# Performance work log

Hardware: AMD Instinct MI355X
Metric: run time of the kernel (lower is better)

Reference implementation:

```python
import jax, jax.numpy as jnp
import numpy as np

N = 100000      # nodes
E = 1600000     # edges (avg degree 16)
DIN = 32
DOUT = 32


def setup_inputs() -> dict:
    key = jax.random.key(0)
    k1, k2, k3 = jax.random.split(key, 3)
    x = jax.random.normal(k1, (N, DIN), dtype=jnp.float32)
    edge_index = jax.random.randint(k2, (2, E), 0, N)  # [2, E] (src, dst)
    W = jax.random.normal(k3, (DIN, DOUT), dtype=jnp.float32) / np.sqrt(DIN).astype(np.float32)
    b = jnp.zeros((DOUT,), dtype=jnp.float32)
    return {"x": x, "edge_index": edge_index, "W": W, "b": b}


def reference(x, edge_index, W, b):
    # GCNConv with norm='both' (DGL GraphConv semantics):
    # out = D_dst^{-1/2} * A * (D_src^{-1/2} * X * W) + b
    src, dst = edge_index[0], edge_index[1]
    ones = jnp.ones((edge_index.shape[1],), dtype=x.dtype)
    out_deg = jax.ops.segment_sum(ones, src, num_segments=N)  # out-degree of src nodes
    in_deg = jax.ops.segment_sum(ones, dst, num_segments=N)   # in-degree of dst nodes
    norm_src = jnp.where(out_deg > 0, out_deg ** -0.5, 0.0)   # [N]
    norm_dst = jnp.where(in_deg > 0, in_deg ** -0.5, 0.0)     # [N]
    # feature transform before aggregation (in_feats >= out_feats path)
    h = (x * norm_src[:, None]) @ W                           # [N, DOUT]
    # sparse neighbor aggregation: gather along src, scatter-add to dst
    agg = jax.ops.segment_sum(h[src], dst, num_segments=N)    # [N, DOUT]
    return agg * norm_dst[:, None] + b
```

## Files before the change

kernel.cpp:

```cpp
#include <hip/hip_runtime.h>
#include <hip/hip_bf16.h>

#define DIN 32
#define DOUT 32
#define BINSHIFT 8
#define BINW 256
#define NBMAX 512
#define PTHREADS 512
#define PK 8
#define PB (PTHREADS * PK)
#define SRCBITS 17
#define SRCMASK ((1u << SRCBITS) - 1u)
#define CAP_LDS 8192
#define AK (CAP_LDS / 1024)

__device__ __forceinline__ float bf_lo(unsigned v) { return __uint_as_float(v << 16); }
__device__ __forceinline__ float bf_hi(unsigned v) { return __uint_as_float(v & 0xffff0000u); }
__device__ __forceinline__ unsigned f2bf_rne(float f) {
    unsigned u = __float_as_uint(f);
    return (u + 0x7fffu + ((u >> 16) & 1u)) >> 16;
}

__global__ void init_caps_kernel(int* __restrict__ baseS, int* __restrict__ baseD,
                                 int* __restrict__ curS, int* __restrict__ curD,
                                 int NB, int cap) {
    int i = threadIdx.x;
    if (i <= NB) {
        int v = i * cap;
        baseS[i] = v; baseD[i] = v;
        if (i < NB) { curS[i] = v; curD[i] = v; }
    }
}

__global__ void hist_coarse_kernel(const int* __restrict__ src, const int* __restrict__ dst,
                                   int E, int* __restrict__ gcntS, int* __restrict__ gcntD) {
    __shared__ int hS[NBMAX], hD[NBMAX];
    for (int i = threadIdx.x; i < NBMAX; i += 256) { hS[i] = 0; hD[i] = 0; }
    __syncthreads();
    int stride = gridDim.x * blockDim.x;
    for (int e = blockIdx.x * blockDim.x + threadIdx.x; e < E; e += stride) {
        atomicAdd(&hS[src[e] >> BINSHIFT], 1);
        atomicAdd(&hD[dst[e] >> BINSHIFT], 1);
    }
    __syncthreads();
    for (int i = threadIdx.x; i < NBMAX; i += 256) {
        if (hS[i]) atomicAdd(&gcntS[i], hS[i]);
        if (hD[i]) atomicAdd(&gcntD[i], hD[i]);
    }
}

__global__ void scan_coarse_kernel(const int* __restrict__ gcntS, const int* __restrict__ gcntD,
                                   int* __restrict__ baseS, int* __restrict__ baseD,
                                   int* __restrict__ curS, int* __restrict__ curD,
                                   int NB, int E) {
    __shared__ int s1[NBMAX], s2[NBMAX];
    int t = threadIdx.x;
    int a = (t < NB) ? gcntS[t] : 0;
    int c = (t < NB) ? gcntD[t] : 0;
    s1[t] = a; s2[t] = c;
    for (int o = 1; o < NBMAX; o <<= 1) {
        __syncthreads();
        int x = (t >= o) ? s1[t - o] : 0;
        int y = (t >= o) ? s2[t - o] : 0;
        __syncthreads();
        s1[t] += x; s2[t] += y;
    }
    __syncthreads();
    if (t < NB) {
        baseS[t] = s1[t] - a; curS[t] = s1[t] - a;
        baseD[t] = s2[t] - c; curD[t] = s2[t] - c;
    }
    if (t == 0) { baseS[NB] = E; baseD[NB] = E; }
}

__global__ void partition_both_kernel(const int* __restrict__ src, const int* __restrict__ dst,
                                      int E, int* __restrict__ curS, int* __restrict__ curD,
                                      int* __restrict__ binnedS, int* __restrict__ binnedD) {
    __shared__ int cntS[NBMAX], cntD[NBMAX];
    __shared__ int gbS[NBMAX], gbD[NBMAX];
    __shared__ int stage[PB];
    __shared__ unsigned short sbin[PB];
    int t = threadIdx.x;
    cntS[t] = 0; cntD[t] = 0;
    __syncthreads();

    int base_e = blockIdx.x * PB;
    int nvalid = E - base_e; if (nvalid > PB) nvalid = PB;

    int vs[PK], vd[PK], rkS[PK], rkD[PK];
#pragma unroll
    for (int i = 0; i < PK; ++i) {
        int e = base_e + i * PTHREADS + t;
        if (e < E) {
            int s = src[e], d = dst[e];
            vs[i] = s; vd[i] = d;
            rkS[i] = atomicAdd(&cntS[s >> BINSHIFT], 1);
            rkD[i] = atomicAdd(&cntD[d >> BINSHIFT], 1);
        } else vs[i] = -1;
    }
    __syncthreads();

    int cS = cntS[t], cD = cntD[t];
    for (int o = 1; o < NBMAX; o <<= 1) {
        __syncthreads();
        int xS = (t >= o) ? cntS[t - o] : 0;
        int xD = (t >= o) ? cntD[t - o] : 0;
        __syncthreads();
        cntS[t] += xS; cntD[t] += xD;
    }
    __syncthreads();
    int lS = cntS[t] - cS, lD = cntD[t] - cD;
    int gS = cS ? atomicAdd(&curS[t], cS) : 0;
    int gD = cD ? atomicAdd(&curD[t], cD) : 0;
    gbS[t] = gS - lS; gbD[t] = gD - lD;
    __syncthreads();
    cntS[t] = lS; cntD[t] = lD;
    __syncthreads();

#pragma unroll
    for (int i = 0; i < PK; ++i) {
        if (vs[i] >= 0) {
            int b = vs[i] >> BINSHIFT;
            int slot = cntS[b] + rkS[i];
            stage[slot] = vs[i];
            sbin[slot] = (unsigned short)b;
        }
    }
    __syncthreads();
    for (int i = t; i < nvalid; i += PTHREADS)
        binnedS[gbS[sbin[i]] + i] = stage[i];
    __syncthreads();

#pragma unroll
    for (int i = 0; i < PK; ++i) {
        if (vs[i] >= 0) {
            int b = vd[i] >> BINSHIFT;
            int slot = cntD[b] + rkD[i];
            stage[slot] = ((vd[i] & (BINW - 1)) << SRCBITS) | vs[i];
            sbin[slot] = (unsigned short)b;
        }
    }
    __syncthreads();
    for (int i = t; i < nvalid; i += PTHREADS)
        binnedD[gbD[sbin[i]] + i] = stage[i];
}

__global__ void cnt_transform_kernel(const int* __restrict__ binnedS,
                                     const int* __restrict__ baseS, const int* __restrict__ endS,
                                     const float* __restrict__ x, const float* __restrict__ W,
                                     unsigned* __restrict__ h, int n) {
    __shared__ int   cnt[BINW];
    __shared__ float Ws[32][33];
    __shared__ float xs[32][33];
    int t = threadIdx.x;
    int b = blockIdx.x;
    int beg = baseS[b], end = endS[b];
    int lo = b << BINSHIFT;

    if (t < BINW) cnt[t] = 0;
    for (int i = t; i < 32 * 32; i += 512) Ws[i >> 5][i & 31] = W[i];
    __syncthreads();
    for (int e = beg + t; e < end; e += 512) atomicAdd(&cnt[binnedS[e] - lo], 1);
    __syncthreads();

    int pr = t & 15, r = t >> 4;
    for (int pass = 0; pass < 8; ++pass) {
        int row = lo + pass * 32 + r;
        if (row < n) {
            float2 xv = *reinterpret_cast<const float2*>(&x[(size_t)row * 32 + 2 * pr]);
            xs[r][2 * pr] = xv.x; xs[r][2 * pr + 1] = xv.y;
        }
        __syncthreads();
        if (row < n) {
            float a0 = 0.f, a1 = 0.f;
#pragma unroll
            for (int k = 0; k < 32; ++k) {
                float xv = xs[r][k];
                a0 += xv * Ws[k][2 * pr];
                a1 += xv * Ws[k][2 * pr + 1];
            }
            int d = cnt[pass * 32 + r];
            float nrm = (d > 0) ? rsqrtf((float)d) : 0.f;
            h[(size_t)row * 16 + pr] = f2bf_rne(a0 * nrm) | (f2bf_rne(a1 * nrm) << 16);
        }
        __syncthreads();
    }
}

__global__ void csr_agg_kernel(const int* __restrict__ binnedD, const int* __restrict__ baseD,
                               const int* __restrict__ endD, const uint4* __restrict__ hb4,
                               const float* __restrict__ bias, float* __restrict__ out, int n) {
    __shared__ int cnt[BINW];
    __shared__ int start[BINW];
    __shared__ int lesrc[CAP_LDS];

    int t = threadIdx.x;
    int b = blockIdx.x;
    int beg = baseD[b], end = endD[b];
    int lo = b << BINSHIFT;
    int q  = t & 3;
    int ng = t >> 2;

    float4 A0 = {0,0,0,0}, A1 = {0,0,0,0};
    float4 B0 = {0,0,0,0}, B1 = {0,0,0,0};
    int deg = 0;

    for (int cb = beg; cb < end; cb += CAP_LDS) {
        int ce = cb + CAP_LDS; if (ce > end) ce = end;
        if (t < BINW) cnt[t] = 0;
        __syncthreads();
        unsigned pv[AK]; int rk[AK];
#pragma unroll
        for (int i = 0; i < AK; ++i) {
            int e = cb + i * 1024 + t;
            if (e < ce) {
                pv[i] = (unsigned)binnedD[e];
                rk[i] = atomicAdd(&cnt[pv[i] >> SRCBITS], 1);
            } else pv[i] = 0xFFFFFFFFu;
        }
        __syncthreads();
        if (t < BINW) start[t] = cnt[t];
        __syncthreads();
        for (int o = 1; o < BINW; o <<= 1) {
            int x = 0;
            if (t < BINW && t >= o) x = start[t - o];
            __syncthreads();
            if (t < BINW) start[t] += x;
            __syncthreads();
        }
        if (t < BINW) start[t] -= cnt[t];
        __syncthreads();
#pragma unroll
        for (int i = 0; i < AK; ++i)
            if (pv[i] != 0xFFFFFFFFu)
                lesrc[start[pv[i] >> SRCBITS] + rk[i]] = (int)(pv[i] & SRCMASK);
        __syncthreads();

        int kb = start[ng], kc = cnt[ng];
        deg += kc;
        int k = kb, ke = kb + kc;
        for (; k + 4 <= ke; k += 4) {
            int s0 = lesrc[k], s1 = lesrc[k + 1], s2 = lesrc[k + 2], s3 = lesrc[k + 3];
            uint4 v0 = hb4[(size_t)s0 * 4 + q];
            uint4 v1 = hb4[(size_t)s1 * 4 + q];
            uint4 v2 = hb4[(size_t)s2 * 4 + q];
            uint4 v3 = hb4[(size_t)s3 * 4 + q];
            A0.x += bf_lo(v0.x); A0.y += bf_hi(v0.x); A0.z += bf_lo(v0.y); A0.w += bf_hi(v0.y);
            A1.x += bf_lo(v0.z); A1.y += bf_hi(v0.z); A1.z += bf_lo(v0.w); A1.w += bf_hi(v0.w);
            B0.x += bf_lo(v1.x); B0.y += bf_hi(v1.x); B0.z += bf_lo(v1.y); B0.w += bf_hi(v1.y);
            B1.x += bf_lo(v1.z); B1.y += bf_hi(v1.z); B1.z += bf_lo(v1.w); B1.w += bf_hi(v1.w);
            A0.x += bf_lo(v2.x); A0.y += bf_hi(v2.x); A0.z += bf_lo(v2.y); A0.w += bf_hi(v2.y);
            A1.x += bf_lo(v2.z); A1.y += bf_hi(v2.z); A1.z += bf_lo(v2.w); A1.w += bf_hi(v2.w);
            B0.x += bf_lo(v3.x); B0.y += bf_hi(v3.x); B0.z += bf_lo(v3.y); B0.w += bf_hi(v3.y);
            B1.x += bf_lo(v3.z); B1.y += bf_hi(v3.z); B1.z += bf_lo(v3.w); B1.w += bf_hi(v3.w);
        }
        for (; k < ke; ++k) {
            uint4 v = hb4[(size_t)lesrc[k] * 4 + q];
            A0.x += bf_lo(v.x); A0.y += bf_hi(v.x); A0.z += bf_lo(v.y); A0.w += bf_hi(v.y);
            A1.x += bf_lo(v.z); A1.y += bf_hi(v.z); A1.z += bf_lo(v.w); A1.w += bf_hi(v.w);
        }
        __syncthreads();
    }

    A0.x += B0.x; A0.y += B0.y; A0.z += B0.z; A0.w += B0.w;
    A1.x += B1.x; A1.y += B1.y; A1.z += B1.z; A1.w += B1.w;

    int node = lo + ng;
    if (node < n) {
        float nrm = (deg > 0) ? rsqrtf((float)deg) : 0.f;
        const float4* b4 = reinterpret_cast<const float4*>(bias);
        float4 bv0 = b4[2 * q], bv1 = b4[2 * q + 1];
        float4 o0, o1;
        o0.x = A0.x * nrm + bv0.x; o0.y = A0.y * nrm + bv0.y;
        o0.z = A0.z * nrm + bv0.z; o0.w = A0.w * nrm + bv0.w;
        o1.x = A1.x * nrm + bv1.x; o1.y = A1.y * nrm + bv1.y;
        o1.z = A1.z * nrm + bv1.z; o1.w = A1.w * nrm + bv1.w;
        float4* o4 = reinterpret_cast<float4*>(out);
        o4[(size_t)node * 8 + 2 * q]     = o0;
        o4[(size_t)node * 8 + 2 * q + 1] = o1;
    }
}

__global__ void deg_kernel(const int* __restrict__ src, const int* __restrict__ dst,
                           int* __restrict__ degs, int* __restrict__ degd, int E) {
    int i = blockIdx.x * blockDim.x + threadIdx.x;
    if (i < E) {
        atomicAdd(&degs[src[i]], 1);
        atomicAdd(&degd[dst[i]], 1);
    }
}

__global__ void transform_f32_kernel(const float* __restrict__ x, const float* __restrict__ W,
                                     const int* __restrict__ degs, float* __restrict__ h, int n) {
    __shared__ float Ws[32][33];
    __shared__ float xs[8][32];
    int col = threadIdx.x & 31;
    int r   = threadIdx.x >> 5;
    for (int i = threadIdx.x; i < 32 * 32; i += 256) Ws[i >> 5][i & 31] = W[i];
    int row = blockIdx.x * 8 + r;
    xs[r][col] = (row < n) ? x[row * 32 + col] : 0.f;
    __syncthreads();
    if (row < n) {
        float acc = 0.f;
#pragma unroll
        for (int k = 0; k < 32; ++k) acc += xs[r][k] * Ws[k][col];
        int d = degs[row];
        float nrm = (d > 0) ? rsqrtf((float)d) : 0.f;
        h[row * 32 + col] = acc * nrm;
    }
}

__global__ void scatter_kernel(const int* __restrict__ src, const int* __restrict__ dst,
                               const float* __restrict__ h, float* __restrict__ out, int E) {
    int t = blockIdx.x * blockDim.x + threadIdx.x;
    int e = t >> 3;
    int q = t & 7;
    if (e < E) {
        int s = src[e];
        int d = dst[e];
        const float4 v = *reinterpret_cast<const float4*>(&h[s * 32 + q * 4]);
        float* o = &out[d * 32 + q * 4];
        atomicAdd(o + 0, v.x);
        atomicAdd(o + 1, v.y);
        atomicAdd(o + 2, v.z);
        atomicAdd(o + 3, v.w);
    }
}

__global__ void finalize_kernel(float* __restrict__ out, const int* __restrict__ degd,
                                const float* __restrict__ b, int n) {
    int t = blockIdx.x * blockDim.x + threadIdx.x;
    if (t < n * 32) {
        int row = t >> 5;
        int col = t & 31;
        int d = degd[row];
        float nrm = (d > 0) ? rsqrtf((float)d) : 0.f;
        out[t] = out[t] * nrm + b[col];
    }
}

extern "C" void kernel_launch(void* const* d_in, const int* in_sizes, int n_in,
                              void* d_out, int out_size, void* d_ws, size_t ws_size,
                              hipStream_t stream) {
    const float* x  = (const float*)d_in[0];
    const int*   ei = (const int*)d_in[1];
    const float* W  = (const float*)d_in[2];
    const float* bb = (const float*)d_in[3];
    float* out = (float*)d_out;

    const int n = in_sizes[0] / DIN;
    const int E = in_sizes[1] / 2;
    const int* src = ei;
    const int* dst = ei + E;

    const int NB = (n + BINW - 1) >> BINSHIFT;

    int cap = (int)((((long long)E / NB) * 3 / 2 + 255) & ~255LL);
    if (cap < 1024) cap = 1024;

    size_t szH      = ((size_t)n * DOUT * sizeof(__hip_bfloat16) + 15) & ~(size_t)15;
    size_t szBinE   = ((size_t)E * sizeof(int) + PB * sizeof(int) + 15) & ~(size_t)15;
    size_t szBinCap = ((size_t)NB * cap * sizeof(int) + PB * sizeof(int) + 15) & ~(size_t)15;

    auto layout = [&](size_t szBin, char* p0, int** binnedS, int** binnedD, unsigned** h,
                      int** gcntS, int** gcntD, int** baseS, int** baseD,
                      int** curS, int** curD) -> size_t {
        char* p = p0;
        *binnedS = (int*)p;       p += szBin;
        *binnedD = (int*)p;       p += szBin;
        *h       = (unsigned*)p;  p += szH;
        *gcntS   = (int*)p;       p += NBMAX * sizeof(int);
        *gcntD   = (int*)p;       p += NBMAX * sizeof(int);
        *baseS   = (int*)p;       p += (NBMAX + 1) * sizeof(int);
        *baseD   = (int*)p;       p += (NBMAX + 1) * sizeof(int);
        *curS    = (int*)p;       p += NBMAX * sizeof(int);
        *curD    = (int*)p;       p += NBMAX * sizeof(int);
        return (size_t)(p - p0);
    };

    int *binnedS, *binnedD, *gcntS, *gcntD, *baseS, *baseD, *curS, *curD;
    unsigned* h;

    const int partBlocks = (E + PB - 1) / PB;
    bool ok = (NB <= NBMAX) && (n <= (1 << SRCBITS));

    if (ok) {
        size_t need = layout(szBinCap, (char*)d_ws, &binnedS, &binnedD, &h,
                             &gcntS, &gcntD, &baseS, &baseD, &curS, &curD);
        if (need <= ws_size) {
            init_caps_kernel<<<1, NBMAX, 0, stream>>>(baseS, baseD, curS, curD, NB, cap);
            partition_both_kernel<<<partBlocks, PTHREADS, 0, stream>>>(src, dst, E, curS, curD,
                                                                       binnedS, binnedD);
            cnt_transform_kernel<<<NB, 512, 0, stream>>>(binnedS, baseS, curS, x, W, h, n);
            csr_agg_kernel<<<NB, 1024, 0, stream>>>(binnedD, baseD, curD, (const uint4*)h,
                                                    bb, out, n);
            return;
        }
        need = layout(szBinE, (char*)d_ws, &binnedS, &binnedD, &h,
                      &gcntS, &gcntD, &baseS, &baseD, &curS, &curD);
        if (need <= ws_size) {
            hipMemsetAsync(gcntS, 0, 2 * NBMAX * sizeof(int), stream);
            hist_coarse_kernel<<<512, 256, 0, stream>>>(src, dst, E, gcntS, gcntD);
            scan_coarse_kernel<<<1, NBMAX, 0, stream>>>(gcntS, gcntD, baseS, baseD,
                                                        curS, curD, NB, E);
            partition_both_kernel<<<partBlocks, PTHREADS, 0, stream>>>(src, dst, E, curS, curD,
                                                                       binnedS, binnedD);
            cnt_transform_kernel<<<NB, 512, 0, stream>>>(binnedS, baseS, curS, x, W, h, n);
            csr_agg_kernel<<<NB, 1024, 0, stream>>>(binnedD, baseD, curD, (const uint4*)h,
                                                    bb, out, n);
            return;
        }
    }

    {
        float* hf   = (float*)d_ws;
        int*   dgs  = (int*)(hf + (size_t)n * DOUT);
        int*   degd = dgs + n;
        hipMemsetAsync(dgs, 0, (size_t)2 * n * sizeof(int), stream);
        hipMemsetAsync(d_out, 0, (size_t)out_size * sizeof(float), stream);
        deg_kernel<<<(E + 255) / 256, 256, 0, stream>>>(src, dst, dgs, degd, E);
        transform_f32_kernel<<<(n + 7) / 8, 256, 0, stream>>>(x, W, dgs, hf, n);
        long long st = (long long)E * 8;
        scatter_kernel<<<(int)((st + 255) / 256), 256, 0, stream>>>(src, dst, hf, out, E);
        finalize_kernel<<<(n * 32 + 255) / 256, 256, 0, stream>>>(out, degd, bb, n);
    }
}
```

Measured before the change: 81.02 us.

## Use wave-shuffle scans and restructure per-bin feature transform

```diff
diff --git a/kernel.cpp b/kernel.cpp
--- a/kernel.cpp
+++ b/kernel.cpp
@@ -20,6 +20,14 @@
     unsigned u = __float_as_uint(f);
     return (u + 0x7fffu + ((u >> 16) & 1u)) >> 16;
 }
+__device__ __forceinline__ int wave_incl_scan(int v) {
+#pragma unroll
+    for (int o = 1; o < 64; o <<= 1) {
+        int u = __shfl_up(v, o, 64);
+        if ((threadIdx.x & 63) >= o) v += u;
+    }
+    return v;
+}
 
 __global__ void init_caps_kernel(int* __restrict__ baseS, int* __restrict__ baseD,
                                  int* __restrict__ curS, int* __restrict__ curD,
@@ -53,22 +61,21 @@
                                    int* __restrict__ baseS, int* __restrict__ baseD,
                                    int* __restrict__ curS, int* __restrict__ curD,
                                    int NB, int E) {
-    __shared__ int s1[NBMAX], s2[NBMAX];
+    __shared__ int wsS[8], wsD[8];
     int t = threadIdx.x;
     int a = (t < NB) ? gcntS[t] : 0;
     int c = (t < NB) ? gcntD[t] : 0;
-    s1[t] = a; s2[t] = c;
-    for (int o = 1; o < NBMAX; o <<= 1) {
-        __syncthreads();
-        int x = (t >= o) ? s1[t - o] : 0;
-        int y = (t >= o) ? s2[t - o] : 0;
-        __syncthreads();
-        s1[t] += x; s2[t] += y;
-    }
-    __syncthreads();
+    int sS = wave_incl_scan(a);
+    int sD = wave_incl_scan(c);
+    int w = t >> 6;
+    if ((t & 63) == 63) { wsS[w] = sS; wsD[w] = sD; }
+    __syncthreads();
+    int addS = 0, addD = 0;
+#pragma unroll
+    for (int i = 0; i < 8; ++i) if (i < w) { addS += wsS[i]; addD += wsD[i]; }
     if (t < NB) {
-        baseS[t] = s1[t] - a; curS[t] = s1[t] - a;
-        baseD[t] = s2[t] - c; curD[t] = s2[t] - c;
+        baseS[t] = sS - a + addS; curS[t] = sS - a + addS;
+        baseD[t] = sD - c + addD; curD[t] = sD - c + addD;
     }
     if (t == 0) { baseS[NB] = E; baseD[NB] = E; }
 }
@@ -78,6 +85,7 @@
                                       int* __restrict__ binnedS, int* __restrict__ binnedD) {
     __shared__ int cntS[NBMAX], cntD[NBMAX];
     __shared__ int gbS[NBMAX], gbD[NBMAX];
+    __shared__ int wsS[8], wsD[8];
     __shared__ int stage[PB];
     __shared__ unsigned short sbin[PB];
     int t = threadIdx.x;
@@ -101,19 +109,18 @@
     __syncthreads();
 
     int cS = cntS[t], cD = cntD[t];
-    for (int o = 1; o < NBMAX; o <<= 1) {
-        __syncthreads();
-        int xS = (t >= o) ? cntS[t - o] : 0;
-        int xD = (t >= o) ? cntD[t - o] : 0;
-        __syncthreads();
-        cntS[t] += xS; cntD[t] += xD;
-    }
-    __syncthreads();
-    int lS = cntS[t] - cS, lD = cntD[t] - cD;
+    int sS = wave_incl_scan(cS);
+    int sD = wave_incl_scan(cD);
+    int w = t >> 6;
+    if ((t & 63) == 63) { wsS[w] = sS; wsD[w] = sD; }
+    __syncthreads();
+    int addS = 0, addD = 0;
+#pragma unroll
+    for (int i = 0; i < 8; ++i) if (i < w) { addS += wsS[i]; addD += wsD[i]; }
+    int lS = sS - cS + addS, lD = sD - cD + addD;
     int gS = cS ? atomicAdd(&curS[t], cS) : 0;
     int gD = cD ? atomicAdd(&curD[t], cD) : 0;
     gbS[t] = gS - lS; gbD[t] = gD - lD;
-    __syncthreads();
     cntS[t] = lS; cntD[t] = lD;
     __syncthreads();
 
@@ -149,9 +156,9 @@
                                      const int* __restrict__ baseS, const int* __restrict__ endS,
                                      const float* __restrict__ x, const float* __restrict__ W,
                                      unsigned* __restrict__ h, int n) {
+    __shared__ float xs[BINW][33];
+    __shared__ float Ws[32][33];
     __shared__ int   cnt[BINW];
-    __shared__ float Ws[32][33];
-    __shared__ float xs[32][33];
     int t = threadIdx.x;
     int b = blockIdx.x;
     int beg = baseS[b], end = endS[b];
@@ -160,30 +167,39 @@
     if (t < BINW) cnt[t] = 0;
     for (int i = t; i < 32 * 32; i += 512) Ws[i >> 5][i & 31] = W[i];
     __syncthreads();
+
     for (int e = beg + t; e < end; e += 512) atomicAdd(&cnt[binnedS[e] - lo], 1);
-    __syncthreads();
-
-    int pr = t & 15, r = t >> 4;
-    for (int pass = 0; pass < 8; ++pass) {
-        int row = lo + pass * 32 + r;
-        if (row < n) {
-            float2 xv = *reinterpret_cast<const float2*>(&x[(size_t)row * 32 + 2 * pr]);
-            xs[r][2 * pr] = xv.x; xs[r][2 * pr + 1] = xv.y;
-        }
-        __syncthreads();
-        if (row < n) {
-            float a0 = 0.f, a1 = 0.f;
-#pragma unroll
-            for (int k = 0; k < 32; ++k) {
-                float xv = xs[r][k];
-                a0 += xv * Ws[k][2 * pr];
-                a1 += xv * Ws[k][2 * pr + 1];
-            }
-            int d = cnt[pass * 32 + r];
-            float nrm = (d > 0) ? rsqrtf((float)d) : 0.f;
-            h[(size_t)row * 16 + pr] = f2bf_rne(a0 * nrm) | (f2bf_rne(a1 * nrm) << 16);
-        }
-        __syncthreads();
+
+    int rcnt = n - lo; if (rcnt > BINW) rcnt = BINW; if (rcnt < 0) rcnt = 0;
+    const float4* x4 = reinterpret_cast<const float4*>(x);
+    for (int i = t; i < rcnt * 8; i += 512) {
+        float4 v = x4[(size_t)lo * 8 + i];
+        int r = i >> 3, c = (i & 7) << 2;
+        xs[r][c] = v.x; xs[r][c + 1] = v.y; xs[r][c + 2] = v.z; xs[r][c + 3] = v.w;
+    }
+    __syncthreads();
+
+    int r = t >> 1, half = t & 1;
+    if (r < rcnt) {
+        float acc[16];
+#pragma unroll
+        for (int j = 0; j < 16; ++j) acc[j] = 0.f;
+#pragma unroll
+        for (int k = 0; k < 32; ++k) {
+            float xv = xs[r][k];
+            const float* wr = &Ws[k][half * 16];
+#pragma unroll
+            for (int j = 0; j < 16; ++j) acc[j] += xv * wr[j];
+        }
+        int d = cnt[r];
+        float nrm = (d > 0) ? rsqrtf((float)d) : 0.f;
+        unsigned o[8];
+#pragma unroll
+        for (int j = 0; j < 8; ++j)
+            o[j] = f2bf_rne(acc[2 * j] * nrm) | (f2bf_rne(acc[2 * j + 1] * nrm) << 16);
+        uint4* h4 = reinterpret_cast<uint4*>(h);
+        h4[(size_t)(lo + r) * 4 + half * 2]     = uint4{o[0], o[1], o[2], o[3]};
+        h4[(size_t)(lo + r) * 4 + half * 2 + 1] = uint4{o[4], o[5], o[6], o[7]};
     }
 }
 
@@ -192,6 +208,7 @@
                                const float* __restrict__ bias, float* __restrict__ out, int n) {
     __shared__ int cnt[BINW];
     __shared__ int start[BINW];
+    __shared__ int wsum[4];
     __shared__ int lesrc[CAP_LDS];
 
     int t = threadIdx.x;
@@ -219,16 +236,20 @@
             } else pv[i] = 0xFFFFFFFFu;
         }
         __syncthreads();
-        if (t < BINW) start[t] = cnt[t];
-        __syncthreads();
-        for (int o = 1; o < BINW; o <<= 1) {
-            int x = 0;
-            if (t < BINW && t >= o) x = start[t - o];
-            __syncthreads();
-            if (t < BINW) start[t] += x;
-            __syncthreads();
-        }
-        if (t < BINW) start[t] -= cnt[t];
+        int v = 0, s = 0;
+        if (t < BINW) {
+            v = cnt[t];
+            s = wave_incl_scan(v);
+            if ((t & 63) == 63) wsum[t >> 6] = s;
+        }
+        __syncthreads();
+        if (t < BINW) {
+            int w = t >> 6, add = 0;
+            if (w > 0) add += wsum[0];
+            if (w > 1) add += wsum[1];
+            if (w > 2) add += wsum[2];
+            start[t] = s - v + add;
+        }
         __syncthreads();
 #pragma unroll
         for (int i = 0; i < AK; ++i)
@@ -255,9 +276,9 @@
             B1.x += bf_lo(v3.z); B1.y += bf_hi(v3.z); B1.z += bf_lo(v3.w); B1.w += bf_hi(v3.w);
         }
         for (; k < ke; ++k) {
-            uint4 v = hb4[(size_t)lesrc[k] * 4 + q];
-            A0.x += bf_lo(v.x); A0.y += bf_hi(v.x); A0.z += bf_lo(v.y); A0.w += bf_hi(v.y);
-            A1.x += bf_lo(v.z); A1.y += bf_hi(v.z); A1.z += bf_lo(v.w); A1.w += bf_hi(v.w);
+            uint4 v4 = hb4[(size_t)lesrc[k] * 4 + q];
+            A0.x += bf_lo(v4.x); A0.y += bf_hi(v4.x); A0.z += bf_lo(v4.y); A0.w += bf_hi(v4.y);
+            A1.x += bf_lo(v4.z); A1.y += bf_hi(v4.z); A1.z += bf_lo(v4.w); A1.w += bf_hi(v4.w);
         }
         __syncthreads();
     }
```

After: 75.26 us (median of 2 runs). 7.1% less time.
